# Optimization experiments

Measured on AMD Instinct MI355X. Metric: run time of the kernel, lower is better.

Reference implementation:

```python
import jax, jax.numpy as jnp
import numpy as np

N_NODES = 100000
DEG = 16
N_EDGES = N_NODES * DEG
D_IN = 64
D_OUT = 64


def setup_inputs() -> dict:
    key = jax.random.key(0)
    k1, k2, k3 = jax.random.split(key, 3)
    X = jax.random.normal(k1, (N_NODES, D_IN), dtype=jnp.float32)
    stdv = 1.0 / np.sqrt(D_OUT)
    weight = jax.random.uniform(k2, (D_IN, D_OUT), dtype=jnp.float32, minval=-stdv, maxval=stdv)
    # CSR: fixed out-degree DEG per node (regularized for reproducible setup)
    row_pointers = (jnp.arange(N_NODES + 1, dtype=jnp.int64) * DEG)
    column_index = jax.random.randint(k3, (N_EDGES,), 0, N_NODES, dtype=jnp.int32)
    # GCN normalization: degrees[i] = 1/sqrt(d_i)
    counts = (row_pointers[1:] - row_pointers[:-1]).astype(jnp.float32)
    degrees = 1.0 / jnp.sqrt(jnp.maximum(counts, 1.0))
    return {"X": X, "weight": weight, "row_pointers": row_pointers,
            "column_index": column_index, "degrees": degrees}


def reference(X, weight, row_pointers, column_index, degrees):
    # Feature transform first (D_OUT <= D_IN keeps aggregation traffic low)
    xw = X @ weight                                   # [N, D_OUT]
    counts = row_pointers[1:] - row_pointers[:-1]     # [N]
    dst = jnp.repeat(jnp.arange(N_NODES, dtype=jnp.int32), counts,
                     total_repeat_length=N_EDGES)     # [E] destination node per edge
    src = column_index                                # [E] neighbor (source) per edge
    norm = degrees[dst] * degrees[src]                # [E] d_i^{-1/2} d_j^{-1/2}
    msgs = xw[src] * norm[:, None]                    # [E, D_OUT]
    out = jax.ops.segment_sum(msgs, dst, num_segments=N_NODES)  # [N, D_OUT]
    return out
```

## Files before the change

### kernel.cpp

```cpp
#include <hip/hip_runtime.h>

#define D 64

static __device__ __forceinline__ unsigned int bf16r(float f) {
    const unsigned int u = __float_as_uint(f);
    return (u + 0x7fffu + ((u >> 16) & 1u)) >> 16;
}

__global__ __launch_bounds__(256, 4)
void gcn_xw_sgpr(const float* __restrict__ X, const float* __restrict__ W,
                 const float* __restrict__ deg, ushort* __restrict__ Y,
                 int n_nodes)
{
    const int lane  = threadIdx.x & 63;
    const int g     = __builtin_amdgcn_readfirstlane((int)(threadIdx.x >> 6));
    const int node  = blockIdx.x * 64 + lane;
    const bool valid = node < n_nodes;

    const float* __restrict__ xrow = X + ((size_t)(valid ? node : 0) << 6);
    const float* __restrict__ wg   = W + 16 * g;

    float acc[16];
#pragma unroll
    for (int f = 0; f < 16; ++f) acc[f] = 0.f;

#pragma unroll
    for (int q = 0; q < 16; ++q) {
        const float4 xv = *(const float4*)(xrow + 4 * q);
#pragma unroll
        for (int j = 0; j < 4; ++j) {
            const float* __restrict__ wr = wg + (size_t)(4 * q + j) * D;
            const float xs = (j == 0) ? xv.x : (j == 1) ? xv.y
                           : (j == 2) ? xv.z : xv.w;
#pragma unroll
            for (int f = 0; f < 16; ++f)
                acc[f] = fmaf(xs, wr[f], acc[f]);
        }
    }

    if (valid) {
        const float dn = deg[node];
        unsigned int r[8];
#pragma unroll
        for (int p = 0; p < 8; ++p)
            r[p] = bf16r(acc[2 * p] * dn) | (bf16r(acc[2 * p + 1] * dn) << 16);
        uint4* dst = (uint4*)(Y + ((size_t)node << 6) + 16 * g);
        dst[0] = make_uint4(r[0], r[1], r[2], r[3]);
        dst[1] = make_uint4(r[4], r[5], r[6], r[7]);
    }
}

__global__ __launch_bounds__(256, 4)
void gcn_gather4(const ushort* __restrict__ Y, const int* __restrict__ rp,
                 const int* __restrict__ col, const float* __restrict__ deg,
                 float* __restrict__ out, int n_nodes)
{
    const int lane   = threadIdx.x & 63;
    const int s      = lane >> 4;
    const int f      = lane & 15;
    const int gwave  = (int)((blockIdx.x * blockDim.x + threadIdx.x) >> 6);
    const int nwaves = (int)((gridDim.x * blockDim.x) >> 6);
    const int ngroups = (n_nodes + 3) >> 2;

    for (int g = gwave; g < ngroups; g += nwaves) {
        const int  n     = g * 4 + s;
        const bool valid = (n < n_nodes);
        const int  rpn   = valid ? rp[n]     : 0;
        const int  rpe   = valid ? rp[n + 1] : 0;
        const int  dcnt  = rpe - rpn;

        const bool ok = !valid || (dcnt == 16 && (rpn & 3) == 0);
        if (__ballot(ok) == ~0ull) {
            int idx[16];
            *(int4*)(idx + 0)  = *(const int4*)(col + rpn + 0);
            *(int4*)(idx + 4)  = *(const int4*)(col + rpn + 4);
            *(int4*)(idx + 8)  = *(const int4*)(col + rpn + 8);
            *(int4*)(idx + 12) = *(const int4*)(col + rpn + 12);

            float a0 = 0.f, a1 = 0.f, a2 = 0.f, a3 = 0.f;
#pragma unroll
            for (int j = 0; j < 16; ++j) {
                const uint2 u = *(const uint2*)(Y + ((size_t)idx[j] << 6) + (f << 2));
                a0 += __uint_as_float(u.x << 16);
                a1 += __uint_as_float(u.x & 0xffff0000u);
                a2 += __uint_as_float(u.y << 16);
                a3 += __uint_as_float(u.y & 0xffff0000u);
            }
            if (valid) {
                const float dn = deg[n];
                float4 v;
                v.x = a0 * dn; v.y = a1 * dn; v.z = a2 * dn; v.w = a3 * dn;
                *(float4*)(out + (size_t)n * D + f * 4) = v;
            }
        } else if (valid) {
            float a0 = 0.f, a1 = 0.f, a2 = 0.f, a3 = 0.f;
            for (int e = rpn; e < rpe; ++e) {
                const int sj = col[e];
                const uint2 u = *(const uint2*)(Y + ((size_t)sj << 6) + (f << 2));
                a0 += __uint_as_float(u.x << 16);
                a1 += __uint_as_float(u.x & 0xffff0000u);
                a2 += __uint_as_float(u.y << 16);
                a3 += __uint_as_float(u.y & 0xffff0000u);
            }
            const float dn = deg[n];
            float4 v;
            v.x = a0 * dn; v.y = a1 * dn; v.z = a2 * dn; v.w = a3 * dn;
            *(float4*)(out + (size_t)n * D + f * 4) = v;
        }
    }
}

static __device__ __forceinline__ float bcast_f(float v, int l) {
    return __uint_as_float(__builtin_amdgcn_readlane(__float_as_uint(v), l));
}

__global__ __launch_bounds__(256, 4)
void gcn_fused_kernel(const float* __restrict__ X, const float* __restrict__ W,
                      const int* __restrict__ rp, const int* __restrict__ col,
                      const float* __restrict__ deg, float* __restrict__ out,
                      int n_nodes)
{
    const int lane   = threadIdx.x & 63;
    const int gwave  = (int)((blockIdx.x * blockDim.x + threadIdx.x) >> 6);
    const int nwaves = (int)((gridDim.x * blockDim.x) >> 6);

    for (int node = gwave; node < n_nodes; node += nwaves) {
        const int start = rp[node];
        const int end   = rp[node + 1];
        const float di  = deg[node];
        float h = 0.f;

        for (int e0 = start; e0 < end; e0 += 64) {
            const int cnt = min(64, end - e0);
            int   s_  = (lane < cnt) ? col[e0 + lane] : 0;
            float nm_ = (lane < cnt) ? di * deg[s_] : 0.f;
            for (int j = 0; j < cnt; ++j) {
                const int   sj = __builtin_amdgcn_readlane(s_, j);
                const float nj = bcast_f(nm_, j);
                h = fmaf(nj, X[(size_t)sj * D + lane], h);
            }
        }

        float c0 = 0.f, c1 = 0.f, c2 = 0.f, c3 = 0.f;
#pragma unroll
        for (int l = 0; l < D; l += 4) {
            c0 = fmaf(bcast_f(h, l + 0), W[(l + 0) * D + lane], c0);
            c1 = fmaf(bcast_f(h, l + 1), W[(l + 1) * D + lane], c1);
            c2 = fmaf(bcast_f(h, l + 2), W[(l + 2) * D + lane], c2);
            c3 = fmaf(bcast_f(h, l + 3), W[(l + 3) * D + lane], c3);
        }
        out[(size_t)node * D + lane] = (c0 + c1) + (c2 + c3);
    }
}

extern "C" void kernel_launch(void* const* d_in, const int* in_sizes, int n_in,
                              void* d_out, int out_size, void* d_ws, size_t ws_size,
                              hipStream_t stream) {
    const float* X   = (const float*)d_in[0];
    const float* W   = (const float*)d_in[1];
    const int*   rp  = (const int*)d_in[2];
    const int*   col = (const int*)d_in[3];
    const float* deg = (const float*)d_in[4];
    float* out = (float*)d_out;

    const int n_nodes = in_sizes[4];
    const size_t y_bytes = (size_t)n_nodes * D * sizeof(ushort);

    if (ws_size >= y_bytes) {
        ushort* Y = (ushort*)d_ws;
        const int k1_blocks = (n_nodes + 63) / 64;
        gcn_xw_sgpr<<<k1_blocks, 256, 0, stream>>>(X, W, deg, Y, n_nodes);
        gcn_gather4<<<2048, 256, 0, stream>>>(Y, rp, col, deg, out, n_nodes);
    } else {
        gcn_fused_kernel<<<1024, 256, 0, stream>>>(X, W, rp, col, deg, out, n_nodes);
    }
}
```

Before: 140.4 us.

## Compute X@W with bf16 MFMA over 16-node strips in persistent waves

Replaces the scalar-FMA feature-transform kernel with a persistent-wave kernel that keeps W in registers as bf16 MFMA B-fragments. Each wave loops over 16-node strips, converts X rows to bf16 and issues 16x16x32 bf16 MFMAs. The aim is to cut the ALU cost of the transform so the first kernel becomes bound by memory bandwidth. In exchange, X and W are rounded to bf16 before the multiply, which lowers accuracy. The output is written as scattered 2-byte stores rather than 16-byte vector stores, which could hurt write efficiency.

```diff
diff --git a/kernel.cpp b/kernel.cpp
--- a/kernel.cpp
+++ b/kernel.cpp
@@ -1,6 +1,15 @@
 #include <hip/hip_runtime.h>
+#include <hip/hip_bf16.h>
 
 #define D 64
+
+typedef __attribute__((ext_vector_type(8))) short bf16x8;
+typedef __attribute__((ext_vector_type(4))) float f32x4;
+
+union Frag {
+    bf16x8 v;
+    __hip_bfloat162 h[4];
+};
 
 static __device__ __forceinline__ unsigned int bf16r(float f) {
     const unsigned int u = __float_as_uint(f);
@@ -8,45 +17,89 @@
 }
 
 __global__ __launch_bounds__(256, 4)
-void gcn_xw_sgpr(const float* __restrict__ X, const float* __restrict__ W,
+void gcn_xw_mfma(const float* __restrict__ X, const float* __restrict__ W,
                  const float* __restrict__ deg, ushort* __restrict__ Y,
-                 int n_nodes)
+                 int n_nodes, int nstrips)
 {
-    const int lane  = threadIdx.x & 63;
-    const int g     = __builtin_amdgcn_readfirstlane((int)(threadIdx.x >> 6));
-    const int node  = blockIdx.x * 64 + lane;
-    const bool valid = node < n_nodes;
-
-    const float* __restrict__ xrow = X + ((size_t)(valid ? node : 0) << 6);
-    const float* __restrict__ wg   = W + 16 * g;
-
-    float acc[16];
-#pragma unroll
-    for (int f = 0; f < 16; ++f) acc[f] = 0.f;
-
-#pragma unroll
-    for (int q = 0; q < 16; ++q) {
-        const float4 xv = *(const float4*)(xrow + 4 * q);
-#pragma unroll
-        for (int j = 0; j < 4; ++j) {
-            const float* __restrict__ wr = wg + (size_t)(4 * q + j) * D;
-            const float xs = (j == 0) ? xv.x : (j == 1) ? xv.y
-                           : (j == 2) ? xv.z : xv.w;
-#pragma unroll
-            for (int f = 0; f < 16; ++f)
-                acc[f] = fmaf(xs, wr[f], acc[f]);
-        }
-    }
-
-    if (valid) {
-        const float dn = deg[node];
-        unsigned int r[8];
-#pragma unroll
-        for (int p = 0; p < 8; ++p)
-            r[p] = bf16r(acc[2 * p] * dn) | (bf16r(acc[2 * p + 1] * dn) << 16);
-        uint4* dst = (uint4*)(Y + ((size_t)node << 6) + 16 * g);
-        dst[0] = make_uint4(r[0], r[1], r[2], r[3]);
-        dst[1] = make_uint4(r[4], r[5], r[6], r[7]);
+    const int lane = threadIdx.x & 63;
+    const int q    = lane >> 4;
+    const int r    = lane & 15;
+    const int wid  = blockIdx.x * 4 + (threadIdx.x >> 6);
+    const int nw   = gridDim.x * 4;
+
+    Frag bf[4][2];
+#pragma unroll
+    for (int ft = 0; ft < 4; ++ft) {
+        const int c = 16 * ft + r;
+#pragma unroll
+        for (int s = 0; s < 2; ++s) {
+            const int k0 = 32 * s + q * 8;
+#pragma unroll
+            for (int p = 0; p < 4; ++p) {
+                const float a = W[(size_t)(k0 + 2 * p)     * D + c];
+                const float b = W[(size_t)(k0 + 2 * p + 1) * D + c];
+                bf[ft][s].h[p] = __float22bfloat162_rn(make_float2(a, b));
+            }
+        }
+    }
+
+    for (int strip = wid; strip < nstrips; strip += nw) {
+        const int n0 = strip * 16;
+        const bool full = (n0 + 16 <= n_nodes);
+
+        Frag af[2];
+        {
+            const int row  = full ? (n0 + r) : min(n0 + r, n_nodes - 1);
+            const float* __restrict__ xr = X + ((size_t)row << 6);
+#pragma unroll
+            for (int s = 0; s < 2; ++s) {
+                const float4 f0 = *(const float4*)(xr + 32 * s + q * 8);
+                const float4 f1 = *(const float4*)(xr + 32 * s + q * 8 + 4);
+                af[s].h[0] = __float22bfloat162_rn(make_float2(f0.x, f0.y));
+                af[s].h[1] = __float22bfloat162_rn(make_float2(f0.z, f0.w));
+                af[s].h[2] = __float22bfloat162_rn(make_float2(f1.x, f1.y));
+                af[s].h[3] = __float22bfloat162_rn(make_float2(f1.z, f1.w));
+            }
+        }
+
+        f32x4 acc[4];
+#pragma unroll
+        for (int ft = 0; ft < 4; ++ft) {
+            f32x4 z = {0.f, 0.f, 0.f, 0.f};
+            acc[ft] = z;
+        }
+#pragma unroll
+        for (int s = 0; s < 2; ++s)
+#pragma unroll
+            for (int ft = 0; ft < 4; ++ft)
+                acc[ft] = __builtin_amdgcn_mfma_f32_16x16x32_bf16(
+                              af[s].v, bf[ft][s].v, acc[ft], 0, 0, 0);
+
+        if (full) {
+            const float4 dn = *(const float4*)(deg + n0 + 4 * q);
+#pragma unroll
+            for (int i = 0; i < 4; ++i) {
+                const int   node = n0 + 4 * q + i;
+                const float d    = (i == 0) ? dn.x : (i == 1) ? dn.y
+                                 : (i == 2) ? dn.z : dn.w;
+                ushort* yr = Y + ((size_t)node << 6) + r;
+#pragma unroll
+                for (int ft = 0; ft < 4; ++ft)
+                    yr[16 * ft] = (ushort)bf16r(acc[ft][i] * d);
+            }
+        } else {
+#pragma unroll
+            for (int i = 0; i < 4; ++i) {
+                const int node = n0 + 4 * q + i;
+                if (node < n_nodes) {
+                    const float d = deg[node];
+                    ushort* yr = Y + ((size_t)node << 6) + r;
+#pragma unroll
+                    for (int ft = 0; ft < 4; ++ft)
+                        yr[16 * ft] = (ushort)bf16r(acc[ft][i] * d);
+                }
+            }
+        }
     }
 }
 
@@ -168,8 +221,8 @@
 
     if (ws_size >= y_bytes) {
         ushort* Y = (ushort*)d_ws;
-        const int k1_blocks = (n_nodes + 63) / 64;
-        gcn_xw_sgpr<<<k1_blocks, 256, 0, stream>>>(X, W, deg, Y, n_nodes);
+        const int nstrips = (n_nodes + 15) / 16;
+        gcn_xw_mfma<<<256, 256, 0, stream>>>(X, W, deg, Y, n_nodes, nstrips);
         gcn_gather4<<<2048, 256, 0, stream>>>(Y, rp, col, deg, out, n_nodes);
     } else {
         gcn_fused_kernel<<<1024, 256, 0, stream>>>(X, W, rp, col, deg, out, n_nodes);
```

After: 120.4 us. -14.2%, faster.
